# Kernel tuning notes

Hardware: AMD Instinct MI355X
Metric: run time of the kernel (lower is better)

The kernel has to match this reference:

```python
import jax, jax.numpy as jnp
import numpy as np

B, S, D_IN, D_OUT = 4, 2048, 1024, 1024


def setup_inputs() -> dict:
    key = jax.random.key(0)
    k1, k2, k3, k4 = jax.random.split(key, 4)
    scale = 1.0 / np.sqrt(D_IN)
    return {
        "x": jax.random.normal(k1, (B, S, D_IN), dtype=jnp.float32),
        # torch nn.Linear weights have shape [d_out, d_in]
        "Wq": jax.random.normal(k2, (D_OUT, D_IN), dtype=jnp.float32) * scale,
        "Wk": jax.random.normal(k3, (D_OUT, D_IN), dtype=jnp.float32) * scale,
        "Wv": jax.random.normal(k4, (D_OUT, D_IN), dtype=jnp.float32) * scale,
    }


def reference(x, Wq, Wk, Wv):
    # Linear projections (torch Linear: y = x @ W.T), no bias
    q = jnp.einsum('bsd,od->bso', x, Wq)
    k = jnp.einsum('bsd,od->bso', x, Wk)
    v = jnp.einsum('bsd,od->bso', x, Wv)
    s = q.shape[1]
    scores = jnp.einsum('bqd,bkd->bqk', q, k)  # [B, S, S]
    causal = jnp.tril(jnp.ones((s, s), dtype=bool))  # True = keep
    scores = jnp.where(causal[None], scores, -jnp.inf)
    scale = jnp.asarray(k.shape[-1], scores.dtype) ** 0.5
    weights = jax.nn.softmax(scores / scale, axis=-1)
    return jnp.einsum('bqk,bkd->bqd', weights, v)
```

## Files before the change

kernel.cpp:

```cpp
#include <hip/hip_runtime.h>

#define BATCH 4
#define SEQ   2048
#define DIM   1024
#define MTOT  (BATCH * SEQ)
#define BK    32

typedef __bf16 bf16x8 __attribute__((ext_vector_type(8)));
typedef __bf16 bf16x4 __attribute__((ext_vector_type(4)));
typedef float  f32x4  __attribute__((ext_vector_type(4)));

__device__ __forceinline__ void gl_lds16(const __bf16* g, __bf16* l) {
    __builtin_amdgcn_global_load_lds(
        (const __attribute__((address_space(1))) void*)g,
        (__attribute__((address_space(3))) void*)l,
        16, 0, 0);
}

__global__ __launch_bounds__(256) void cvt_all_kernel(
    const float* __restrict__ x,  const float* __restrict__ w0,
    const float* __restrict__ w1, const float* __restrict__ w2,
    __bf16* __restrict__ xd, __bf16* __restrict__ d0,
    __bf16* __restrict__ d1, __bf16* __restrict__ d2,
    float* __restrict__ sums)
{
    const int bid = blockIdx.x;
    if (bid >= 5632) {
        const int i = ((bid - 5632) * 256 + threadIdx.x) * 4;
        *(float4*)(sums + i) = (float4){0.f, 0.f, 0.f, 0.f};
        return;
    }
    const float* s;
    __bf16* d;
    int base;
    if (bid < 4096)      { s = x;  d = xd; base = bid; }
    else if (bid < 4608) { s = w0; d = d0; base = bid - 4096; }
    else if (bid < 5120) { s = w1; d = d1; base = bid - 4608; }
    else                 { s = w2; d = d2; base = bid - 5120; }
    const int i = (base * 256 + threadIdx.x) * 8;
    const float4 a = *(const float4*)(s + i);
    const float4 b = *(const float4*)(s + i + 4);
    bf16x8 o;
    o[0] = (__bf16)a.x; o[1] = (__bf16)a.y; o[2] = (__bf16)a.z; o[3] = (__bf16)a.w;
    o[4] = (__bf16)b.x; o[5] = (__bf16)b.y; o[6] = (__bf16)b.z; o[7] = (__bf16)b.w;
    *(bf16x8*)(d + i) = o;
}

__device__ __forceinline__ void gemm_core(
    const __bf16* __restrict__ A, size_t lda,
    const __bf16* __restrict__ Bm, size_t ldb,
    int m0, int n0, int kTiles,
    __bf16* lA, __bf16* lB,
    f32x4 (&acc)[4][4])
{
    const int tid  = threadIdx.x;
    const int lane = tid & 63;
    const int wave = tid >> 6;
    const int wm = (wave >> 1) << 6;
    const int wn = (wave & 1) << 6;

#pragma unroll
    for (int i = 0; i < 4; ++i)
#pragma unroll
        for (int j = 0; j < 4; ++j)
            acc[i][j] = (f32x4){0.f, 0.f, 0.f, 0.f};

    for (int kt = 0; kt < kTiles; ++kt) {
        const int k0 = kt << 5;
        __syncthreads();
#pragma unroll
        for (int it = 0; it < 2; ++it) {
            const int f   = tid + (it << 8);
            const int row = f >> 2;
            const int col = (f & 3) << 3;
            gl_lds16(A  + (size_t)(m0 + row) * lda + (size_t)(k0 + col), lA + f * 8);
            gl_lds16(Bm + (size_t)(n0 + row) * ldb + (size_t)(k0 + col), lB + f * 8);
        }
        __syncthreads();

        bf16x8 af[4], bfr[4];
#pragma unroll
        for (int i = 0; i < 4; ++i) {
            af[i]  = *(const bf16x8*)(lA + (size_t)(wm + i * 16 + (lane & 15)) * BK + ((lane >> 4) << 3));
            bfr[i] = *(const bf16x8*)(lB + (size_t)(wn + i * 16 + (lane & 15)) * BK + ((lane >> 4) << 3));
        }
#pragma unroll
        for (int i = 0; i < 4; ++i)
#pragma unroll
            for (int j = 0; j < 4; ++j)
                acc[i][j] = __builtin_amdgcn_mfma_f32_16x16x32_bf16(af[i], bfr[j], acc[i][j], 0, 0, 0);
    }
}

__device__ __forceinline__ void store_tile_bf16(
    f32x4 (&acc)[4][4], __bf16* scratch, bool transpose, float scale,
    __bf16* dst, size_t ldo, size_t r0, size_t c0,
    bool expMask = false, bool diag = false, float* sums = nullptr)
{
    const int tid  = threadIdx.x;
    const int lane = tid & 63;
    const int wave = tid >> 6;
    const int wm = (wave >> 1) << 6, wn = (wave & 1) << 6;
    const int quad = lane >> 4;
    const int ln15 = lane & 15;

#pragma unroll
    for (int p = 0; p < 4; ++p) {
        __syncthreads();
        if (!transpose) {
            if (wm == ((p >> 1) << 6)) {
#pragma unroll
                for (int ih = 0; ih < 2; ++ih) {
                    const int i = ((p & 1) << 1) + ih;
                    const int lr = ih * 16 + quad * 4;
#pragma unroll
                    for (int r = 0; r < 4; ++r) {
                        const int lm = wm + ((p & 1) << 5) + lr + r;
                        float ps = 0.f;
#pragma unroll
                        for (int j = 0; j < 4; ++j) {
                            const int ln = wn + j * 16 + ln15;
                            float v = acc[i][j][r] * scale;
                            if (expMask) {
                                v = (!diag || ln <= lm) ? __expf(v) : 0.f;
                            }
                            const __bf16 vb = (__bf16)v;
                            scratch[(lr + r) * 136 + ln] = vb;
                            ps += (float)vb;
                        }
                        if (sums) {
#pragma unroll
                            for (int off = 1; off < 16; off <<= 1)
                                ps += __shfl_xor(ps, off);
                            if (ln15 == 0)
                                atomicAdd(&sums[r0 + (p << 5) + lr + r], ps);
                        }
                    }
                }
            }
        } else {
            if (wn == ((p >> 1) << 6)) {
#pragma unroll
                for (int jh = 0; jh < 2; ++jh) {
                    const int j = ((p & 1) << 1) + jh;
                    const int lr = jh * 16 + ln15;
#pragma unroll
                    for (int i = 0; i < 4; ++i)
#pragma unroll
                        for (int r = 0; r < 4; ++r)
                            scratch[lr * 136 + wm + i * 16 + quad * 4 + r] =
                                (__bf16)(acc[i][j][r] * scale);
                }
            }
        }
        __syncthreads();
#pragma unroll
        for (int it = 0; it < 2; ++it) {
            const int g   = tid + (it << 8);
            const int row = g >> 4;
            const int col = (g & 15) << 3;
            *(bf16x8*)(dst + (r0 + p * 32 + row) * ldo + c0 + col) =
                *(const bf16x8*)(scratch + row * 136 + col);
        }
    }
}

__global__ __launch_bounds__(512, 2) void qkv_kernel(
    const __bf16* __restrict__ x,
    const __bf16* __restrict__ Wq,
    const __bf16* __restrict__ Wk,
    const __bf16* __restrict__ Wv,
    __bf16* __restrict__ Q, __bf16* __restrict__ Kb, __bf16* __restrict__ Vt)
{
    __shared__ __bf16 smem[49152];

    const int L  = blockIdx.x;
    const int g  = (L & 7) * 32 + (L >> 3);
    const int m0 = (g >> 3) << 8;
    const int B3 = g & 7;

    const int tid  = threadIdx.x;
    const int lane = tid & 63;
    const int ln15 = lane & 15;
    const int quad = lane >> 4;
    const int wave = tid >> 6;
    const int wm   = wave >> 2;
    const int wn   = wave & 3;

    const int r0  = tid >> 3;
    const int cst = ((((tid & 7) + 8) - (r0 & 7)) & 7) << 3;
    const int cq  = (((quad << 3) + ((ln15 & 7) << 3)) & 63);

    int aoff[4];
#pragma unroll
    for (int i = 0; i < 4; ++i) aoff[i] = ((wm << 6) + i * 16 + ln15) * 64 + cq;
    const int boff = (wn * 16 + ln15) * 64 + cq;

    const __bf16* Ab = x + (size_t)m0 * DIM;
    const int nt = DIM / 64;

    for (int uu = 0; uu < 3; ++uu) {
        const int u  = B3 * 3 + uu;
        const int z  = u >> 3;
        const int nh = u & 7;
        const int n0 = nh << 7;
        const __bf16* W  = (z == 0) ? Wq : (z == 1) ? Wk : Wv;
        const __bf16* Bb = W + (size_t)n0 * DIM;

        f32x4 acc[8][2];
#pragma unroll
        for (int i = 0; i < 8; ++i)
#pragma unroll
            for (int j = 0; j < 2; ++j) acc[i][j] = (f32x4){0.f, 0.f, 0.f, 0.f};

#define SA(h, t) do {                                                         \
    const __bf16* gs_ = Ab + (size_t)((h) * 128 + r0) * DIM + ((t) << 6) + cst; \
    __bf16* ls_ = smem + (((t) & 1) * 24576 + (h) * 8192) + tid * 8;          \
    gl_lds16(gs_, ls_);                                                       \
    gl_lds16(gs_ + (size_t)64 * DIM, ls_ + 4096); } while (0)
#define SB(h, t) do {                                                         \
    const __bf16* gs_ = Bb + (size_t)((h) * 64 + r0) * DIM + ((t) << 6) + cst; \
    __bf16* ls_ = smem + (((t) & 1) * 24576 + 16384 + (h) * 4096) + tid * 8;  \
    gl_lds16(gs_, ls_); } while (0)

        bf16x8 aF[4][2], bF[2][2];
#define LOAD_A(h) do { const __bf16* p_ = smem + cb_ * 24576 + (h) * 8192;    \
    _Pragma("unroll") for (int i_ = 0; i_ < 4; ++i_) {                        \
        aF[i_][0] = *(const bf16x8*)(p_ + aoff[i_]);                          \
        aF[i_][1] = *(const bf16x8*)(p_ + (aoff[i_] ^ 32)); } } while (0)
#define LOAD_B(s, h) do {                                                     \
    const __bf16* p_ = smem + cb_ * 24576 + 16384 + (h) * 4096;               \
    bF[s][0] = *(const bf16x8*)(p_ + boff);                                   \
    bF[s][1] = *(const bf16x8*)(p_ + (boff ^ 32)); } while (0)
#define MFMA_Q(mh, nhb, s) do {                                               \
    __builtin_amdgcn_s_setprio(1);                                            \
    _Pragma("unroll") for (int i_ = 0; i_ < 4; ++i_) {                        \
        acc[(mh)*4+i_][nhb] = __builtin_amdgcn_mfma_f32_16x16x32_bf16(        \
            aF[i_][0], bF[s][0], acc[(mh)*4+i_][nhb], 0, 0, 0);               \
        acc[(mh)*4+i_][nhb] = __builtin_amdgcn_mfma_f32_16x16x32_bf16(        \
            aF[i_][1], bF[s][1], acc[(mh)*4+i_][nhb], 0, 0, 0); }             \
    __builtin_amdgcn_s_setprio(0); } while (0)

        SA(0, 0);
        SB(0, 0);
        SB(1, 0);
        SA(1, 0);
        SA(0, 1);
        SB(0, 1);
        asm volatile("s_waitcnt vmcnt(3)" ::: "memory");
        __builtin_amdgcn_s_barrier();

        for (int T = 0; T < nt; ++T) {
            const int cb_ = T & 1;
            LOAD_A(0); LOAD_B(0, 0);
            if (T + 1 < nt) SB(1, T + 1);
            __builtin_amdgcn_s_barrier();
            MFMA_Q(0, 0, 0);
            __builtin_amdgcn_s_barrier();
            LOAD_B(1, 1);
            if (T + 1 < nt) SA(1, T + 1);
            __builtin_amdgcn_s_barrier();
            MFMA_Q(0, 1, 1);
            __builtin_amdgcn_s_barrier();
            LOAD_A(1);
            if (T + 2 < nt) SA(0, T + 2);
            __builtin_amdgcn_s_barrier();
            MFMA_Q(1, 1, 1);
            __builtin_amdgcn_s_barrier();
            if (T + 2 < nt) {
                SB(0, T + 2);
                asm volatile("s_waitcnt vmcnt(3)" ::: "memory");
            } else if (T + 1 < nt) {
                asm volatile("s_waitcnt vmcnt(0)" ::: "memory");
            }
            __builtin_amdgcn_s_barrier();
            MFMA_Q(1, 0, 0);
            __builtin_amdgcn_s_barrier();
        }
#undef SA
#undef SB
#undef LOAD_A
#undef LOAD_B
#undef MFMA_Q

        __syncthreads();
        __bf16* scratch = smem;

        if (z < 2) {
            __bf16* dst = (z == 0) ? Q : Kb;
#pragma unroll
            for (int h = 0; h < 2; ++h) {
#pragma unroll
                for (int i = 0; i < 4; ++i) {
                    const int lr = wm * 64 + i * 16 + quad * 4;
#pragma unroll
                    for (int nhb = 0; nhb < 2; ++nhb) {
                        const int lc = nhb * 64 + wn * 16 + ln15;
#pragma unroll
                        for (int r = 0; r < 4; ++r)
                            scratch[(lr + r) * 136 + lc] = (__bf16)acc[h * 4 + i][nhb][r];
                    }
                }
                __syncthreads();
#pragma unroll
                for (int it = 0; it < 4; ++it) {
                    const int f = tid + (it << 9);
                    const int row = f >> 4, col = (f & 15) << 3;
                    *(bf16x8*)(dst + (size_t)(m0 + h * 128 + row) * DIM + n0 + col) =
                        *(const bf16x8*)(scratch + row * 136 + col);
                }
                __syncthreads();
            }
        } else {
            const size_t b  = (size_t)(m0 >> 11);
            const int  ms0  = m0 & (SEQ - 1);
            __bf16* dst = Vt + b * (size_t)DIM * SEQ;
#pragma unroll
            for (int mh = 0; mh < 2; ++mh)
#pragma unroll
                for (int i = 0; i < 4; ++i) {
                    const int sl = mh * 128 + wm * 64 + i * 16 + quad * 4;
#pragma unroll
                    for (int nhb = 0; nhb < 2; ++nhb) {
                        const int dl = nhb * 64 + wn * 16 + ln15;
                        bf16x4 v;
#pragma unroll
                        for (int r = 0; r < 4; ++r) v[r] = (__bf16)acc[mh * 4 + i][nhb][r];
                        *(bf16x4*)(scratch + dl * 264 + sl) = v;
                    }
                }
            __syncthreads();
#pragma unroll
            for (int it = 0; it < 8; ++it) {
                const int f = tid + (it << 9);
                const int row = f >> 5, blk = f & 31;
                *(bf16x8*)(dst + (size_t)(n0 + row) * SEQ + ms0 + blk * 8) =
                    *(const bf16x8*)(scratch + row * 264 + blk * 8);
            }
            __syncthreads();
        }
    }
}

__global__ __launch_bounds__(256) void scores_kernel(
    const __bf16* __restrict__ Q, const __bf16* __restrict__ Kb,
    __bf16* __restrict__ Sc, float* __restrict__ sums)
{
    const int L = blockIdx.x;
    const int g = (L & 7) * 68 + (L >> 3);
    const int b = g / 136;
    const int t = g - b * 136;
    int i = (int)((sqrtf(8.f * t + 1.f) - 1.f) * 0.5f);
    while ((i + 1) * (i + 2) / 2 <= t) ++i;
    while (i * (i + 1) / 2 > t) --i;
    const int j = t - i * (i + 1) / 2;

    __shared__ __bf16 smem[8192];
    __bf16* lA = smem;
    __bf16* lB = smem + 128 * BK;
    const __bf16* A  = Q  + (size_t)b * SEQ * DIM;
    const __bf16* Bm = Kb + (size_t)b * SEQ * DIM;

    f32x4 acc[4][4];
    gemm_core(A, DIM, Bm, DIM, i << 7, j << 7, DIM / BK, lA, lB, acc);

    store_tile_bf16(acc, smem, false, 0.03125f,
                    Sc + (size_t)b * SEQ * SEQ, SEQ,
                    (size_t)(i << 7), (size_t)(j << 7),
                    true, (i == j),
                    sums + (size_t)b * SEQ);
}

__global__ __launch_bounds__(256) void pv_kernel(
    const __bf16* __restrict__ P, const __bf16* __restrict__ Vt,
    const float* __restrict__ sums, float* __restrict__ out)
{
    const int L = blockIdx.x;
    const int c = L & 7;
    const int k = L >> 3;
    const int b = c >> 1;
    const int i = 15 - (c & 1) - ((k >> 3) << 1);
    const int x = k & 7;

    __shared__ __bf16 smem[8192];
    __bf16* lA = smem;
    __bf16* lB = smem + 128 * BK;
    const __bf16* A  = P  + (size_t)b * SEQ * SEQ;
    const __bf16* Bm = Vt + (size_t)b * DIM * SEQ;

    f32x4 acc[4][4];
    gemm_core(A, SEQ, Bm, SEQ, i << 7, x << 7, (i + 1) * (128 / BK), lA, lB, acc);

    const int lane = threadIdx.x & 63;
    const int wave = threadIdx.x >> 6;
    const int wm = (wave >> 1) << 6, wn = (wave & 1) << 6;
#pragma unroll
    for (int ii = 0; ii < 4; ++ii)
#pragma unroll
        for (int jj = 0; jj < 4; ++jj)
#pragma unroll
            for (int r = 0; r < 4; ++r) {
                const int m = (i << 7) + wm + ii * 16 + ((lane >> 4) << 2) + r;
                const int n = (x << 7) + wn + jj * 16 + (lane & 15);
                out[((size_t)b * SEQ + m) * DIM + n] =
                    acc[ii][jj][r] / sums[(b << 11) + m];
            }
}

extern "C" void kernel_launch(void* const* d_in, const int* in_sizes, int n_in,
                              void* d_out, int out_size, void* d_ws, size_t ws_size,
                              hipStream_t stream) {
    const float* x  = (const float*)d_in[0];
    const float* Wq = (const float*)d_in[1];
    const float* Wk = (const float*)d_in[2];
    const float* Wv = (const float*)d_in[3];
    float* out = (float*)d_out;

    char* ws = (char*)d_ws;
    __bf16* Q  = (__bf16*)(ws);
    __bf16* Kb = (__bf16*)(ws + (16ull << 20));
    __bf16* Vt = (__bf16*)(ws + (32ull << 20));
    __bf16* Sc = (__bf16*)(ws + (48ull << 20));
    __bf16* Wqb = (__bf16*)(ws + (80ull << 20));
    __bf16* Wkb = (__bf16*)(ws + (82ull << 20));
    __bf16* Wvb = (__bf16*)(ws + (84ull << 20));
    float*  sums = (float*)(ws + (86ull << 20));
    __bf16* xb  = (__bf16*)d_out;

    cvt_all_kernel<<<dim3(5640), 256, 0, stream>>>(x, Wq, Wk, Wv, xb, Wqb, Wkb, Wvb, sums);

    qkv_kernel    <<<dim3(256),  512, 0, stream>>>(xb, Wqb, Wkb, Wvb, Q, Kb, Vt);
    scores_kernel <<<dim3(544),  256, 0, stream>>>(Q, Kb, Sc, sums);
    pv_kernel     <<<dim3(512),  256, 0, stream>>>(Sc, Vt, sums, out);
}
```

Measured before the change: 230.3 us.

## Remap QKV GEMM waves to 64x64 subtiles and software-pipeline A fragments

Changes the 8-wave layout in the QKV projection kernel from 2x4 (each wave 128x32) to 4x2 (each wave 64x64). This raises the MFMA-to-LDS-read ratio per wave, so each A fragment is reused across four B columns. The main loop is rewritten with double-buffered A register fragments (aFa/aFb), unrolled by two, and the LDS read for the next tile is interleaved with the current MFMA groups using retuned vmcnt waits. The cost is more register pressure from extra fragment buffers and a more fragile wait/barrier schedule.

```diff
diff --git a/kernel.cpp b/kernel.cpp
--- a/kernel.cpp
+++ b/kernel.cpp
@@ -9,6 +9,8 @@
 typedef __bf16 bf16x8 __attribute__((ext_vector_type(8)));
 typedef __bf16 bf16x4 __attribute__((ext_vector_type(4)));
 typedef float  f32x4  __attribute__((ext_vector_type(4)));
+
+#define VMCNT(N) asm volatile("s_waitcnt vmcnt(" #N ")" ::: "memory")
 
 __device__ __forceinline__ void gl_lds16(const __bf16* g, __bf16* l) {
     __builtin_amdgcn_global_load_lds(
@@ -184,8 +186,8 @@
     const int ln15 = lane & 15;
     const int quad = lane >> 4;
     const int wave = tid >> 6;
-    const int wm   = wave >> 2;
-    const int wn   = wave & 3;
+    const int wm   = wave >> 1;
+    const int wn   = wave & 1;
 
     const int r0  = tid >> 3;
     const int cst = ((((tid & 7) + 8) - (r0 & 7)) & 7) << 3;
@@ -193,25 +195,28 @@
 
     int aoff[4];
 #pragma unroll
-    for (int i = 0; i < 4; ++i) aoff[i] = ((wm << 6) + i * 16 + ln15) * 64 + cq;
-    const int boff = (wn * 16 + ln15) * 64 + cq;
+    for (int i = 0; i < 4; ++i)
+        aoff[i] = ((wm >> 1) ? 8192 : 0) + (((wm & 1) << 6) + i * 16 + ln15) * 64 + cq;
+    int boff[4];
+#pragma unroll
+    for (int j = 0; j < 4; ++j)
+        boff[j] = 16384 + (wn ? 4096 : 0) + (j * 16 + ln15) * 64 + cq;
 
     const __bf16* Ab = x + (size_t)m0 * DIM;
-    const int nt = DIM / 64;
+    constexpr int nt = DIM / 64;
 
     for (int uu = 0; uu < 3; ++uu) {
         const int u  = B3 * 3 + uu;
         const int z  = u >> 3;
-        const int nh = u & 7;
-        const int n0 = nh << 7;
+        const int n0 = (u & 7) << 7;
         const __bf16* W  = (z == 0) ? Wq : (z == 1) ? Wk : Wv;
         const __bf16* Bb = W + (size_t)n0 * DIM;
 
-        f32x4 acc[8][2];
-#pragma unroll
-        for (int i = 0; i < 8; ++i)
-#pragma unroll
-            for (int j = 0; j < 2; ++j) acc[i][j] = (f32x4){0.f, 0.f, 0.f, 0.f};
+        f32x4 acc[4][4];
+#pragma unroll
+        for (int i = 0; i < 4; ++i)
+#pragma unroll
+            for (int j = 0; j < 4; ++j) acc[i][j] = (f32x4){0.f, 0.f, 0.f, 0.f};
 
 #define SA(h, t) do {                                                         \
     const __bf16* gs_ = Ab + (size_t)((h) * 128 + r0) * DIM + ((t) << 6) + cst; \
@@ -223,65 +228,77 @@
     __bf16* ls_ = smem + (((t) & 1) * 24576 + 16384 + (h) * 4096) + tid * 8;  \
     gl_lds16(gs_, ls_); } while (0)
 
-        bf16x8 aF[4][2], bF[2][2];
-#define LOAD_A(h) do { const __bf16* p_ = smem + cb_ * 24576 + (h) * 8192;    \
-    _Pragma("unroll") for (int i_ = 0; i_ < 4; ++i_) {                        \
-        aF[i_][0] = *(const bf16x8*)(p_ + aoff[i_]);                          \
-        aF[i_][1] = *(const bf16x8*)(p_ + (aoff[i_] ^ 32)); } } while (0)
-#define LOAD_B(s, h) do {                                                     \
-    const __bf16* p_ = smem + cb_ * 24576 + 16384 + (h) * 4096;               \
-    bF[s][0] = *(const bf16x8*)(p_ + boff);                                   \
-    bF[s][1] = *(const bf16x8*)(p_ + (boff ^ 32)); } while (0)
-#define MFMA_Q(mh, nhb, s) do {                                               \
+        bf16x8 aFa[4][2], aFb[4][2], bFr[2][2];
+#define LDA_LO(DST, t) do { const __bf16* p_ = smem + ((t) & 1) * 24576;      \
+    DST[0][0] = *(const bf16x8*)(p_ + aoff[0]);                               \
+    DST[0][1] = *(const bf16x8*)(p_ + (aoff[0] ^ 32));                        \
+    DST[1][0] = *(const bf16x8*)(p_ + aoff[1]);                               \
+    DST[1][1] = *(const bf16x8*)(p_ + (aoff[1] ^ 32)); } while (0)
+#define LDA_HI(DST, t) do { const __bf16* p_ = smem + ((t) & 1) * 24576;      \
+    DST[2][0] = *(const bf16x8*)(p_ + aoff[2]);                               \
+    DST[2][1] = *(const bf16x8*)(p_ + (aoff[2] ^ 32));                        \
+    DST[3][0] = *(const bf16x8*)(p_ + aoff[3]);                               \
+    DST[3][1] = *(const bf16x8*)(p_ + (aoff[3] ^ 32)); } while (0)
+#define LDB(s, j, t) do { const __bf16* p_ = smem + ((t) & 1) * 24576;        \
+    bFr[s][0] = *(const bf16x8*)(p_ + boff[j]);                               \
+    bFr[s][1] = *(const bf16x8*)(p_ + (boff[j] ^ 32)); } while (0)
+#define MG(j, s, AC) do {                                                     \
     __builtin_amdgcn_s_setprio(1);                                            \
     _Pragma("unroll") for (int i_ = 0; i_ < 4; ++i_) {                        \
-        acc[(mh)*4+i_][nhb] = __builtin_amdgcn_mfma_f32_16x16x32_bf16(        \
-            aF[i_][0], bF[s][0], acc[(mh)*4+i_][nhb], 0, 0, 0);               \
-        acc[(mh)*4+i_][nhb] = __builtin_amdgcn_mfma_f32_16x16x32_bf16(        \
-            aF[i_][1], bF[s][1], acc[(mh)*4+i_][nhb], 0, 0, 0); }             \
+        acc[i_][j] = __builtin_amdgcn_mfma_f32_16x16x32_bf16(                 \
+            AC[i_][0], bFr[s][0], acc[i_][j], 0, 0, 0);                       \
+        acc[i_][j] = __builtin_amdgcn_mfma_f32_16x16x32_bf16(                 \
+            AC[i_][1], bFr[s][1], acc[i_][j], 0, 0, 0); }                     \
     __builtin_amdgcn_s_setprio(0); } while (0)
 
-        SA(0, 0);
-        SB(0, 0);
-        SB(1, 0);
-        SA(1, 0);
-        SA(0, 1);
-        SB(0, 1);
-        asm volatile("s_waitcnt vmcnt(3)" ::: "memory");
+#define TILE(AC, AN, T) do {                                                  \
+                       \
+    LDB(1, 1, T);                                                             \
+    if ((T) + 1 < nt) SB(0, (T) + 1);                                         \
+    __builtin_amdgcn_s_barrier();                                             \
+    MG(0, 0, AC);                                                             \
+    __builtin_amdgcn_s_barrier();                                             \
+      \
+    LDB(0, 2, T);                                                             \
+    if ((T) + 1 < nt) SB(1, (T) + 1);                                         \
+    if ((T) + 2 < nt) SA(0, (T) + 2);                                         \
+    if ((T) + 1 < nt) { if ((T) + 2 < nt) VMCNT(4); else VMCNT(2); }          \
+    __builtin_amdgcn_s_barrier();                                             \
+    MG(1, 1, AC);                                                             \
+    __builtin_amdgcn_s_barrier();                                             \
+      \
+    LDB(1, 3, T);                                                             \
+    if ((T) + 1 < nt) LDA_LO(AN, (T) + 1);                                    \
+    if ((T) + 2 < nt) SA(1, (T) + 2);                                         \
+    if ((T) + 1 < nt) { if ((T) + 2 < nt) VMCNT(5); else VMCNT(1); }          \
+    __builtin_amdgcn_s_barrier();                                             \
+    MG(2, 0, AC);                                                             \
+    __builtin_amdgcn_s_barrier();                                             \
+           \
+    if ((T) + 1 < nt) { LDA_HI(AN, (T) + 1); LDB(0, 0, (T) + 1); }            \
+    if ((T) + 1 < nt) { if ((T) + 2 < nt) VMCNT(4); else VMCNT(0); }          \
+    __builtin_amdgcn_s_barrier();                                             \
+    MG(3, 1, AC);                                                             \
+    __builtin_amdgcn_s_barrier(); } while (0)
+
+        SA(0, 0); SA(1, 0); SB(0, 0); SB(1, 0);
+        SA(0, 1); SA(1, 1);
+        VMCNT(4);
         __builtin_amdgcn_s_barrier();
-
-        for (int T = 0; T < nt; ++T) {
-            const int cb_ = T & 1;
-            LOAD_A(0); LOAD_B(0, 0);
-            if (T + 1 < nt) SB(1, T + 1);
-            __builtin_amdgcn_s_barrier();
-            MFMA_Q(0, 0, 0);
-            __builtin_amdgcn_s_barrier();
-            LOAD_B(1, 1);
-            if (T + 1 < nt) SA(1, T + 1);
-            __builtin_amdgcn_s_barrier();
-            MFMA_Q(0, 1, 1);
-            __builtin_amdgcn_s_barrier();
-            LOAD_A(1);
-            if (T + 2 < nt) SA(0, T + 2);
-            __builtin_amdgcn_s_barrier();
-            MFMA_Q(1, 1, 1);
-            __builtin_amdgcn_s_barrier();
-            if (T + 2 < nt) {
-                SB(0, T + 2);
-                asm volatile("s_waitcnt vmcnt(3)" ::: "memory");
-            } else if (T + 1 < nt) {
-                asm volatile("s_waitcnt vmcnt(0)" ::: "memory");
-            }
-            __builtin_amdgcn_s_barrier();
-            MFMA_Q(1, 0, 0);
-            __builtin_amdgcn_s_barrier();
+        LDA_LO(aFa, 0); LDA_HI(aFa, 0); LDB(0, 0, 0);
+
+#pragma unroll 1
+        for (int T = 0; T < nt; T += 2) {
+            TILE(aFa, aFb, T);
+            TILE(aFb, aFa, T + 1);
         }
 #undef SA
 #undef SB
-#undef LOAD_A
-#undef LOAD_B
-#undef MFMA_Q
+#undef LDA_LO
+#undef LDA_HI
+#undef LDB
+#undef MG
+#undef TILE
 
         __syncthreads();
         __bf16* scratch = smem;
@@ -290,15 +307,17 @@
             __bf16* dst = (z == 0) ? Q : Kb;
 #pragma unroll
             for (int h = 0; h < 2; ++h) {
-#pragma unroll
-                for (int i = 0; i < 4; ++i) {
-                    const int lr = wm * 64 + i * 16 + quad * 4;
-#pragma unroll
-                    for (int nhb = 0; nhb < 2; ++nhb) {
-                        const int lc = nhb * 64 + wn * 16 + ln15;
-#pragma unroll
-                        for (int r = 0; r < 4; ++r)
-                            scratch[(lr + r) * 136 + lc] = (__bf16)acc[h * 4 + i][nhb][r];
+                if ((wm >> 1) == h) {
+#pragma unroll
+                    for (int i = 0; i < 4; ++i) {
+                        const int lr = ((wm & 1) << 6) + i * 16 + quad * 4;
+#pragma unroll
+                        for (int j = 0; j < 4; ++j) {
+                            const int lc = (wn << 6) + j * 16 + ln15;
+#pragma unroll
+                            for (int r = 0; r < 4; ++r)
+                                scratch[(lr + r) * 136 + lc] = (__bf16)acc[i][j][r];
+                        }
                     }
                 }
                 __syncthreads();
@@ -316,19 +335,17 @@
             const int  ms0  = m0 & (SEQ - 1);
             __bf16* dst = Vt + b * (size_t)DIM * SEQ;
 #pragma unroll
-            for (int mh = 0; mh < 2; ++mh)
-#pragma unroll
-                for (int i = 0; i < 4; ++i) {
-                    const int sl = mh * 128 + wm * 64 + i * 16 + quad * 4;
-#pragma unroll
-                    for (int nhb = 0; nhb < 2; ++nhb) {
-                        const int dl = nhb * 64 + wn * 16 + ln15;
-                        bf16x4 v;
-#pragma unroll
-                        for (int r = 0; r < 4; ++r) v[r] = (__bf16)acc[mh * 4 + i][nhb][r];
-                        *(bf16x4*)(scratch + dl * 264 + sl) = v;
-                    }
+            for (int i = 0; i < 4; ++i) {
+                const int sl = (wm << 6) + i * 16 + quad * 4;
+#pragma unroll
+                for (int j = 0; j < 4; ++j) {
+                    const int dl = (wn << 6) + j * 16 + ln15;
+                    bf16x4 v;
+#pragma unroll
+                    for (int r = 0; r < 4; ++r) v[r] = (__bf16)acc[i][j][r];
+                    *(bf16x4*)(scratch + dl * 264 + sl) = v;
                 }
+            }
             __syncthreads();
 #pragma unroll
             for (int it = 0; it < 8; ++it) {
```

After: 230.9 us. About the same (+0.3%).
